# Performance work log

Measured on AMD Instinct MI355X. Metric: run time of the kernel, lower is better.

The kernel has to match this reference:

```python
import jax, jax.numpy as jnp
import numpy as np
from jax import lax

L, B, T = 512, 1024, 48


def setup_inputs() -> dict:
    key = jax.random.key(0)
    k1, k2, k3, k4, k5 = jax.random.split(key, 5)
    emissions = jax.random.normal(k1, (L, B, T), dtype=jnp.float32)
    tags = jax.random.randint(k2, (L, B), 0, T)
    mask = jnp.ones((L, B), dtype=bool)
    start_transitions = jax.random.uniform(k3, (T,), minval=-0.1, maxval=0.1, dtype=jnp.float32)
    end_transitions = jax.random.uniform(k4, (T,), minval=-0.1, maxval=0.1, dtype=jnp.float32)
    transitions = jax.random.uniform(k5, (T, T), minval=-0.1, maxval=0.1, dtype=jnp.float32)
    return {
        'emissions': emissions,
        'tags': tags,
        'mask': mask,
        'start_transitions': start_transitions,
        'end_transitions': end_transitions,
        'transitions': transitions,
    }


def reference(emissions, tags, mask, start_transitions, end_transitions, transitions):
    # emissions: [L, B, T] float; tags: [L, B] int; mask: [L, B] bool (seq-first)
    fm = mask.astype(emissions.dtype)
    seq_len, batch, _ = emissions.shape
    b_idx = jnp.arange(batch)

    # ---- numerator: score of the gold path ----
    # emission score at each step: emissions[i, b, tags[i, b]] -> [L, B]
    em_sc = jnp.take_along_axis(emissions, tags[:, :, None], axis=2)[:, :, 0]
    # transition score between consecutive tags -> [L-1, B]
    trans_sc = transitions[tags[:-1], tags[1:]]
    score = start_transitions[tags[0]] + em_sc[0]
    score = score + jnp.sum((trans_sc + em_sc[1:]) * fm[1:], axis=0)
    seq_ends = mask.astype(jnp.int32).sum(axis=0) - 1  # [B]
    last_tags = tags[seq_ends, b_idx]
    score = score + end_transitions[last_tags]

    # ---- denominator: log partition via forward algorithm (scan) ----
    alpha0 = start_transitions + emissions[0]  # [B, T]

    def step(alpha, xs):
        em, m = xs  # em: [B, T], m: [B]
        # [B, T(prev), T(next)] logsumexp over prev
        next_alpha = jax.nn.logsumexp(
            alpha[:, :, None] + transitions[None, :, :] + em[:, None, :], axis=1)
        alpha = jnp.where(m[:, None], next_alpha, alpha)
        return alpha, None

    alpha, _ = lax.scan(step, alpha0, (emissions[1:], mask[1:]))
    denominator = jax.nn.logsumexp(alpha + end_transitions, axis=1)  # [B]

    llh = score - denominator
    return jnp.mean(llh)  # reduction='mean' (default)
```

## Files before the change

kernel.cpp:

```cpp
#include <hip/hip_runtime.h>

#define LSEQ 512
#define BATCH 1024
#define T 48

typedef __fp16 h2_t __attribute__((ext_vector_type(2)));

static __device__ __forceinline__ float bcast_lane0(float x) {
    return __int_as_float(__builtin_amdgcn_readfirstlane(__float_as_int(x)));
}

static __device__ __forceinline__ float dot2acc(int pk_bits, h2_t e, float acc) {
#if __has_builtin(__builtin_amdgcn_fdot2)
    return __builtin_amdgcn_fdot2(__builtin_bit_cast(h2_t, pk_bits), e, acc, false);
#else
    h2_t a = __builtin_bit_cast(h2_t, pk_bits);
    return __builtin_fmaf((float)a.x, (float)e.x,
           __builtin_fmaf((float)a.y, (float)e.y, acc));
#endif
}

static __device__ __forceinline__ float fast_rcp(float x) {
#if __has_builtin(__builtin_amdgcn_rcpf)
    return __builtin_amdgcn_rcpf(x);
#else
    return 1.0f / x;
#endif
}

static __device__ __forceinline__ int pack_pairs(float w) {
    int wsh = __builtin_amdgcn_update_dpp(0, __float_as_int(w), 0x111, 0xF, 0xF, true);
    return __builtin_bit_cast(int, __builtin_amdgcn_cvt_pkrtz(w, __int_as_float(wsh)));
}

__global__ __launch_bounds__(256, 1) void crf_forward(
    const float* __restrict__ emissions,
    const int* __restrict__ mask,
    const float* __restrict__ start_tr,
    const float* __restrict__ end_tr,
    const float* __restrict__ trans,
    float* __restrict__ denom_out)
{
    const int wave = threadIdx.x >> 6;
    const int lane = threadIdx.x & 63;
    const int b    = blockIdx.x * 4 + wave;
    const bool valid = (lane < T);
    const int jc   = valid ? lane : (T - 1);

    h2_t Ep[T / 2];
    #pragma unroll
    for (int k = 0; k < T / 2; ++k) {
        float e0 = __expf(trans[(2 * k) * T + jc]);
        float e1 = __expf(trans[(2 * k + 1) * T + jc]);
        Ep[k] = __builtin_amdgcn_cvt_pkrtz(e0, e1);
    }

    const float a0 = start_tr[jc] + emissions[(size_t)b * T + jc];
    const float A0 = bcast_lane0(a0);
    float w = valid ? __expf(a0 - A0) : 0.f;
    float C = A0;
    int pk = pack_pairs(w);

    float em0_ = emissions[((size_t)1 * BATCH + b) * T + jc];
    float em1_ = emissions[((size_t)2 * BATCH + b) * T + jc];
    float em2_ = emissions[((size_t)3 * BATCH + b) * T + jc];
    float em3_ = emissions[((size_t)4 * BATCH + b) * T + jc];
    int   mk0_ = mask[1 * BATCH + b];
    int   mk1_ = mask[2 * BATCH + b];
    int   mk2_ = mask[3 * BATCH + b];
    int   mk3_ = mask[4 * BATCH + b];

    for (int t = 1; t <= LSEQ - 1; ++t) {
        const float em = em0_;  em0_ = em1_; em1_ = em2_; em2_ = em3_;
        const int   mk = mk0_;  mk0_ = mk1_; mk1_ = mk2_; mk2_ = mk3_;
        int tn = t + 4; if (tn > LSEQ - 1) tn = LSEQ - 1;
        em3_ = emissions[((size_t)tn * BATCH + b) * T + jc];
        mk3_ = mask[tn * BATCH + b];

        const float em0 = bcast_lane0(em);
        const float e   = __expf(em - em0);

        float acc0 = 0.f, acc1 = 0.f, acc2 = 0.f, acc3 = 0.f;
        #pragma unroll
        for (int k = 0; k < T / 2; k += 4) {
            acc0 = dot2acc(__builtin_amdgcn_readlane(pk, 2 * k + 0), Ep[k + 0], acc0);
            acc1 = dot2acc(__builtin_amdgcn_readlane(pk, 2 * k + 2), Ep[k + 1], acc1);
            acc2 = dot2acc(__builtin_amdgcn_readlane(pk, 2 * k + 4), Ep[k + 2], acc2);
            acc3 = dot2acc(__builtin_amdgcn_readlane(pk, 2 * k + 6), Ep[k + 3], acc3);
        }
        const float S  = (acc0 + acc1) + (acc2 + acc3);
        const float S0 = bcast_lane0(S);
        const float rs = fast_rcp(S0);
        const float lg = __logf(S0);
        const float wnew = (e * rs) * S;

        const bool upd = (mk != 0);
        w = (upd && valid) ? wnew : w;
        C = upd ? (C + em0 + lg) : C;

        pk = pack_pairs(w);
    }

    float v = valid ? (w * __expf(end_tr[jc])) : 0.f;
    #pragma unroll
    for (int off = 32; off > 0; off >>= 1) v += __shfl_xor(v, off);
    if (lane == 0) denom_out[b] = C + __logf(v);
}

__global__ __launch_bounds__(256) void crf_score_partial(
    const float* __restrict__ emissions,
    const int* __restrict__ tags,
    const int* __restrict__ mask,
    const float* __restrict__ trans,
    float* __restrict__ part,
    int* __restrict__ cnt,
    int csz)
{
    const int gid = blockIdx.x * blockDim.x + threadIdx.x;
    const int b = gid & (BATCH - 1);
    const int c = gid >> 10;
    const int t0 = c * csz;
    const int t1 = t0 + csz;

    float sc = 0.f;
    int ct = 0;
    const int tstart = (t0 == 0) ? 1 : t0;
    if (t0 == 0) ct += mask[b] ? 1 : 0;

    int tag_prev = tags[(tstart - 1) * BATCH + b];
    for (int t = tstart; t < t1; ++t) {
        const int tag = tags[t * BATCH + b];
        const int mt = mask[t * BATCH + b];
        if (mt) {
            sc += trans[tag_prev * T + tag]
                + emissions[((size_t)t * BATCH + b) * T + tag];
            ct += 1;
        }
        tag_prev = tag;
    }
    part[gid] = sc;
    cnt[gid] = ct;
}

__global__ __launch_bounds__(1024) void crf_combine(
    const float* __restrict__ emissions,
    const int* __restrict__ tags,
    const float* __restrict__ start_tr,
    const float* __restrict__ end_tr,
    const float* __restrict__ part,
    const int* __restrict__ cnt,
    const float* __restrict__ denom,
    float* __restrict__ out,
    int nchunk)
{
    const int b = threadIdx.x;

    const int tag0 = tags[b];
    float sc = start_tr[tag0] + emissions[(size_t)b * T + tag0];
    int ct = 0;
    for (int c = 0; c < nchunk; ++c) {
        sc += part[c * BATCH + b];
        ct += cnt[c * BATCH + b];
    }
    if (ct < 1) ct = 1;
    const int last_tag = tags[(ct - 1) * BATCH + b];
    sc += end_tr[last_tag];

    const float llh = sc - denom[b];

    __shared__ float red[1024];
    red[b] = llh;
    __syncthreads();
    #pragma unroll
    for (int s = 512; s > 0; s >>= 1) {
        if (b < s) red[b] += red[b + s];
        __syncthreads();
    }
    if (b == 0) out[0] = red[0] / (float)BATCH;
}

extern "C" void kernel_launch(void* const* d_in, const int* in_sizes, int n_in,
                              void* d_out, int out_size, void* d_ws, size_t ws_size,
                              hipStream_t stream) {
    const float* emissions        = (const float*)d_in[0];
    const int* tags               = (const int*)d_in[1];
    const int* mask               = (const int*)d_in[2];
    const float* start_tr         = (const float*)d_in[3];
    const float* end_tr           = (const float*)d_in[4];
    const float* trans            = (const float*)d_in[5];
    float* out                    = (float*)d_out;

    const int nchunk = (ws_size >= (size_t)(BATCH * 4 + 32 * BATCH * 8 + 64)) ? 32 : 8;
    const int csz    = LSEQ / nchunk;

    float* denom = (float*)d_ws;
    float* part  = denom + BATCH;
    int*   cnt   = (int*)(part + nchunk * BATCH);

    crf_forward<<<256, 256, 0, stream>>>(emissions, mask, start_tr, end_tr, trans, denom);
    crf_score_partial<<<nchunk * BATCH / 256, 256, 0, stream>>>(
        emissions, tags, mask, trans, part, cnt, csz);
    crf_combine<<<1, 1024, 0, stream>>>(emissions, tags, start_tr, end_tr,
                                        part, cnt, denom, out, nchunk);
}
```

Before: 198.0 us.

## Use fp32 FMA with LDS-resident exp(transitions) and chunked double-buffered emission prefetch

Replaces the packed-fp16 dot2 inner product with fp32 FMAs that read exp(transitions) from a padded transposed table in LDS instead of registers. Emission and mask loads become double-buffered chunks of 8 timesteps, prefetched one chunk ahead. The aim is to restore fp32 precision and hide global load latency better, at the cost of 48 LDS reads per step on top of the 48 readlanes, which may lengthen the serial per-step critical path.

```diff
diff --git a/kernel.cpp b/kernel.cpp
--- a/kernel.cpp
+++ b/kernel.cpp
@@ -3,23 +3,16 @@
 #define LSEQ 512
 #define BATCH 1024
 #define T 48
-
-typedef __fp16 h2_t __attribute__((ext_vector_type(2)));
+#define TP 49
+#define CHUNK 8
+#define NCH (LSEQ / CHUNK)
 
 static __device__ __forceinline__ float bcast_lane0(float x) {
     return __int_as_float(__builtin_amdgcn_readfirstlane(__float_as_int(x)));
 }
-
-static __device__ __forceinline__ float dot2acc(int pk_bits, h2_t e, float acc) {
-#if __has_builtin(__builtin_amdgcn_fdot2)
-    return __builtin_amdgcn_fdot2(__builtin_bit_cast(h2_t, pk_bits), e, acc, false);
-#else
-    h2_t a = __builtin_bit_cast(h2_t, pk_bits);
-    return __builtin_fmaf((float)a.x, (float)e.x,
-           __builtin_fmaf((float)a.y, (float)e.y, acc));
-#endif
-}
-
+static __device__ __forceinline__ float rl(float x, int i) {
+    return __int_as_float(__builtin_amdgcn_readlane(__float_as_int(x), i));
+}
 static __device__ __forceinline__ float fast_rcp(float x) {
 #if __has_builtin(__builtin_amdgcn_rcpf)
     return __builtin_amdgcn_rcpf(x);
@@ -28,9 +21,28 @@
 #endif
 }
 
-static __device__ __forceinline__ int pack_pairs(float w) {
-    int wsh = __builtin_amdgcn_update_dpp(0, __float_as_int(w), 0x111, 0xF, 0xF, true);
-    return __builtin_bit_cast(int, __builtin_amdgcn_cvt_pkrtz(w, __int_as_float(wsh)));
+static __device__ __forceinline__ void crf_step(
+    float& w, float& C, float em, int mk, int tt, bool valid,
+    const float* __restrict__ Ejv)
+{
+    const float em0 = bcast_lane0(em);
+    const float e   = __expf(em - em0);
+    float s0 = 0.f, s1 = 0.f, s2 = 0.f, s3 = 0.f;
+    #pragma unroll
+    for (int i = 0; i < T; i += 4) {
+        s0 = __builtin_fmaf(rl(w, i + 0), Ejv[i + 0], s0);
+        s1 = __builtin_fmaf(rl(w, i + 1), Ejv[i + 1], s1);
+        s2 = __builtin_fmaf(rl(w, i + 2), Ejv[i + 2], s2);
+        s3 = __builtin_fmaf(rl(w, i + 3), Ejv[i + 3], s3);
+    }
+    const float S    = (s0 + s1) + (s2 + s3);
+    const float S0   = bcast_lane0(S);
+    const float rs   = fast_rcp(S0);
+    const float lg   = __logf(S0);
+    const float wnew = (e * rs) * S;
+    const bool  upd  = (mk != 0) && (tt < LSEQ);
+    w = (upd && valid) ? wnew : w;
+    C = upd ? (C + em0 + lg) : C;
 }
 
 __global__ __launch_bounds__(256, 1) void crf_forward(
@@ -41,64 +53,78 @@
     const float* __restrict__ trans,
     float* __restrict__ denom_out)
 {
-    const int wave = threadIdx.x >> 6;
-    const int lane = threadIdx.x & 63;
+    __shared__ float Elds[T * TP];
+    const int tid = threadIdx.x;
+    #pragma unroll
+    for (int r = 0; r < (T * T + 255) / 256; ++r) {
+        int g = tid + r * 256;
+        if (g < T * T) {
+            int i = g / T, j = g % T;
+            Elds[j * TP + i] = __expf(trans[g]);
+        }
+    }
+    __syncthreads();
+
+    const int wave = tid >> 6, lane = tid & 63;
     const int b    = blockIdx.x * 4 + wave;
     const bool valid = (lane < T);
     const int jc   = valid ? lane : (T - 1);
-
-    h2_t Ep[T / 2];
-    #pragma unroll
-    for (int k = 0; k < T / 2; ++k) {
-        float e0 = __expf(trans[(2 * k) * T + jc]);
-        float e1 = __expf(trans[(2 * k + 1) * T + jc]);
-        Ep[k] = __builtin_amdgcn_cvt_pkrtz(e0, e1);
-    }
-
-    const float a0 = start_tr[jc] + emissions[(size_t)b * T + jc];
+    const unsigned ebase = (unsigned)(jc * TP);
+
+    const float* emb = emissions + (size_t)b * T + jc;
+    const int*   mkb = mask + b;
+
+    const float a0 = start_tr[jc] + emb[0];
     const float A0 = bcast_lane0(a0);
     float w = valid ? __expf(a0 - A0) : 0.f;
     float C = A0;
-    int pk = pack_pairs(w);
-
-    float em0_ = emissions[((size_t)1 * BATCH + b) * T + jc];
-    float em1_ = emissions[((size_t)2 * BATCH + b) * T + jc];
-    float em2_ = emissions[((size_t)3 * BATCH + b) * T + jc];
-    float em3_ = emissions[((size_t)4 * BATCH + b) * T + jc];
-    int   mk0_ = mask[1 * BATCH + b];
-    int   mk1_ = mask[2 * BATCH + b];
-    int   mk2_ = mask[3 * BATCH + b];
-    int   mk3_ = mask[4 * BATCH + b];
-
-    for (int t = 1; t <= LSEQ - 1; ++t) {
-        const float em = em0_;  em0_ = em1_; em1_ = em2_; em2_ = em3_;
-        const int   mk = mk0_;  mk0_ = mk1_; mk1_ = mk2_; mk2_ = mk3_;
-        int tn = t + 4; if (tn > LSEQ - 1) tn = LSEQ - 1;
-        em3_ = emissions[((size_t)tn * BATCH + b) * T + jc];
-        mk3_ = mask[tn * BATCH + b];
-
-        const float em0 = bcast_lane0(em);
-        const float e   = __expf(em - em0);
-
-        float acc0 = 0.f, acc1 = 0.f, acc2 = 0.f, acc3 = 0.f;
-        #pragma unroll
-        for (int k = 0; k < T / 2; k += 4) {
-            acc0 = dot2acc(__builtin_amdgcn_readlane(pk, 2 * k + 0), Ep[k + 0], acc0);
-            acc1 = dot2acc(__builtin_amdgcn_readlane(pk, 2 * k + 2), Ep[k + 1], acc1);
-            acc2 = dot2acc(__builtin_amdgcn_readlane(pk, 2 * k + 4), Ep[k + 2], acc2);
-            acc3 = dot2acc(__builtin_amdgcn_readlane(pk, 2 * k + 6), Ep[k + 3], acc3);
-        }
-        const float S  = (acc0 + acc1) + (acc2 + acc3);
-        const float S0 = bcast_lane0(S);
-        const float rs = fast_rcp(S0);
-        const float lg = __logf(S0);
-        const float wnew = (e * rs) * S;
-
-        const bool upd = (mk != 0);
-        w = (upd && valid) ? wnew : w;
-        C = upd ? (C + em0 + lg) : C;
-
-        pk = pack_pairs(w);
+
+    float emA[CHUNK], emB[CHUNK];
+    int   mkA[CHUNK], mkB[CHUNK];
+    #pragma unroll
+    for (int u = 0; u < CHUNK; ++u) {
+        const int tt = 1 + u;
+        emA[u] = emb[(size_t)tt * (BATCH * T)];
+        mkA[u] = mkb[tt * BATCH];
+    }
+
+    for (int c = 0; c < NCH; c += 2) {
+        {
+            const int tB = 1 + (c + 1) * CHUNK;
+            #pragma unroll
+            for (int u = 0; u < CHUNK; ++u) {
+                int tt = tB + u; if (tt > LSEQ - 1) tt = LSEQ - 1;
+                emB[u] = emb[(size_t)tt * (BATCH * T)];
+                mkB[u] = mkb[tt * BATCH];
+            }
+        }
+        {
+            const int t0 = 1 + c * CHUNK;
+            #pragma unroll
+            for (int u = 0; u < CHUNK; ++u) {
+                unsigned eb = ebase;
+                asm volatile("" : "+v"(eb));
+                crf_step(w, C, emA[u], mkA[u], t0 + u, valid, &Elds[eb]);
+            }
+        }
+        {
+            const int tA = 1 + (c + 2) * CHUNK;
+            #pragma unroll
+            for (int u = 0; u < CHUNK; ++u) {
+                int tt = tA + u; if (tt > LSEQ - 1) tt = LSEQ - 1;
+                emA[u] = emb[(size_t)tt * (BATCH * T)];
+                mkA[u] = mkb[tt * BATCH];
+            }
+        }
+        {
+            const int t0 = 1 + (c + 1) * CHUNK;
+            #pragma unroll
+            for (int u = 0; u < CHUNK; ++u) {
+                unsigned eb = ebase;
+                asm volatile("" : "+v"(eb));
+                crf_step(w, C, emB[u], mkB[u], t0 + u, valid, &Elds[eb]);
+            }
+        }
     }
 
     float v = valid ? (w * __expf(end_tr[jc])) : 0.f;
```

Result: slower. 224.9 us (+13.6%).

## Batch 16 sequences per wave and compute CRF forward recursion with MFMA

Applied to the files above, without the earlier changes.

The forward-algorithm kernel now processes 16 batch elements per 64-lane wave and performs the 48x48 transition matrix-vector products as 16x16x16 fp16 MFMA ops instead of per-lane dot2 with readlane broadcasts. Rescaling switches from a lane-0 reference to the per-column max, applied after the emission exponent, and the emission loads become vectorized float4 loads with a 4-slot software prefetch. This cuts the number of waves from 1024 to 64 and removes the serial readlane chain, at the cost of 9 dependent MFMAs per step and lower occupancy and parallelism across the GPU.

```diff
diff --git a/kernel.cpp b/kernel.cpp
--- a/kernel.cpp
+++ b/kernel.cpp
@@ -4,36 +4,45 @@
 #define BATCH 1024
 #define T 48
 
-typedef __fp16 h2_t __attribute__((ext_vector_type(2)));
-
-static __device__ __forceinline__ float bcast_lane0(float x) {
-    return __int_as_float(__builtin_amdgcn_readfirstlane(__float_as_int(x)));
-}
-
-static __device__ __forceinline__ float dot2acc(int pk_bits, h2_t e, float acc) {
-#if __has_builtin(__builtin_amdgcn_fdot2)
-    return __builtin_amdgcn_fdot2(__builtin_bit_cast(h2_t, pk_bits), e, acc, false);
+typedef float f4 __attribute__((ext_vector_type(4)));
+typedef __fp16 h2 __attribute__((ext_vector_type(2)));
+typedef __fp16 h4 __attribute__((ext_vector_type(4)));
+typedef float f32x4 __attribute__((ext_vector_type(4)));
+
+static __device__ __forceinline__ f32x4 mfma16(h4 a, h4 b, f32x4 c) {
+#if defined(__HIP_DEVICE_COMPILE__)
+#if __has_builtin(__builtin_amdgcn_mfma_f32_16x16x16f16)
+    return __builtin_amdgcn_mfma_f32_16x16x16f16(a, b, c, 0, 0, 0);
 #else
-    h2_t a = __builtin_bit_cast(h2_t, pk_bits);
-    return __builtin_fmaf((float)a.x, (float)e.x,
-           __builtin_fmaf((float)a.y, (float)e.y, acc));
+    return __builtin_amdgcn_mfma_f32_16x16x16_f16(a, b, c, 0, 0, 0);
 #endif
-}
-
+#else
+    return c;
+#endif
+}
+
+static __device__ __forceinline__ h4 pack4(float a, float b, float c, float d) {
+    h2 lo = __builtin_amdgcn_cvt_pkrtz(a, b);
+    h2 hi = __builtin_amdgcn_cvt_pkrtz(c, d);
+    h4 r; r.x = lo.x; r.y = lo.y; r.z = hi.x; r.w = hi.y;
+    return r;
+}
+static __device__ __forceinline__ h4 sel4(bool c, h4 a, h4 b) {
+    int2 ai = __builtin_bit_cast(int2, a), bi = __builtin_bit_cast(int2, b);
+    int2 r; r.x = c ? ai.x : bi.x; r.y = c ? ai.y : bi.y;
+    return __builtin_bit_cast(h4, r);
+}
 static __device__ __forceinline__ float fast_rcp(float x) {
-#if __has_builtin(__builtin_amdgcn_rcpf)
+#if defined(__HIP_DEVICE_COMPILE__) && __has_builtin(__builtin_amdgcn_rcpf)
     return __builtin_amdgcn_rcpf(x);
 #else
     return 1.0f / x;
 #endif
 }
 
-static __device__ __forceinline__ int pack_pairs(float w) {
-    int wsh = __builtin_amdgcn_update_dpp(0, __float_as_int(w), 0x111, 0xF, 0xF, true);
-    return __builtin_bit_cast(int, __builtin_amdgcn_cvt_pkrtz(w, __int_as_float(wsh)));
-}
-
-__global__ __launch_bounds__(256, 1) void crf_forward(
+struct Slot { f4 em[3]; int mk; };
+
+__global__ __launch_bounds__(64, 1) void crf_forward(
     const float* __restrict__ emissions,
     const int* __restrict__ mask,
     const float* __restrict__ start_tr,
@@ -41,70 +50,106 @@
     const float* __restrict__ trans,
     float* __restrict__ denom_out)
 {
-    const int wave = threadIdx.x >> 6;
-    const int lane = threadIdx.x & 63;
-    const int b    = blockIdx.x * 4 + wave;
-    const bool valid = (lane < T);
-    const int jc   = valid ? lane : (T - 1);
-
-    h2_t Ep[T / 2];
-    #pragma unroll
-    for (int k = 0; k < T / 2; ++k) {
-        float e0 = __expf(trans[(2 * k) * T + jc]);
-        float e1 = __expf(trans[(2 * k + 1) * T + jc]);
-        Ep[k] = __builtin_amdgcn_cvt_pkrtz(e0, e1);
-    }
-
-    const float a0 = start_tr[jc] + emissions[(size_t)b * T + jc];
-    const float A0 = bcast_lane0(a0);
-    float w = valid ? __expf(a0 - A0) : 0.f;
-    float C = A0;
-    int pk = pack_pairs(w);
-
-    float em0_ = emissions[((size_t)1 * BATCH + b) * T + jc];
-    float em1_ = emissions[((size_t)2 * BATCH + b) * T + jc];
-    float em2_ = emissions[((size_t)3 * BATCH + b) * T + jc];
-    float em3_ = emissions[((size_t)4 * BATCH + b) * T + jc];
-    int   mk0_ = mask[1 * BATCH + b];
-    int   mk1_ = mask[2 * BATCH + b];
-    int   mk2_ = mask[3 * BATCH + b];
-    int   mk3_ = mask[4 * BATCH + b];
-
-    for (int t = 1; t <= LSEQ - 1; ++t) {
-        const float em = em0_;  em0_ = em1_; em1_ = em2_; em2_ = em3_;
-        const int   mk = mk0_;  mk0_ = mk1_; mk1_ = mk2_; mk2_ = mk3_;
-        int tn = t + 4; if (tn > LSEQ - 1) tn = LSEQ - 1;
-        em3_ = emissions[((size_t)tn * BATCH + b) * T + jc];
-        mk3_ = mask[tn * BATCH + b];
-
-        const float em0 = bcast_lane0(em);
-        const float e   = __expf(em - em0);
-
-        float acc0 = 0.f, acc1 = 0.f, acc2 = 0.f, acc3 = 0.f;
-        #pragma unroll
-        for (int k = 0; k < T / 2; k += 4) {
-            acc0 = dot2acc(__builtin_amdgcn_readlane(pk, 2 * k + 0), Ep[k + 0], acc0);
-            acc1 = dot2acc(__builtin_amdgcn_readlane(pk, 2 * k + 2), Ep[k + 1], acc1);
-            acc2 = dot2acc(__builtin_amdgcn_readlane(pk, 2 * k + 4), Ep[k + 2], acc2);
-            acc3 = dot2acc(__builtin_amdgcn_readlane(pk, 2 * k + 6), Ep[k + 3], acc3);
+    const int lane  = threadIdx.x;
+    const int col   = lane & 15;
+    const int g     = lane >> 4;
+    const int bbase = blockIdx.x * 16;
+    const int b     = bbase + col;
+
+    h4 Af[3][3];
+    #pragma unroll
+    for (int rb = 0; rb < 3; ++rb)
+        #pragma unroll
+        for (int kc = 0; kc < 3; ++kc) {
+            float e0 = __expf(trans[(16*kc + 4*g + 0)*T + 16*rb + col]);
+            float e1 = __expf(trans[(16*kc + 4*g + 1)*T + 16*rb + col]);
+            float e2 = __expf(trans[(16*kc + 4*g + 2)*T + 16*rb + col]);
+            float e3 = __expf(trans[(16*kc + 4*g + 3)*T + 16*rb + col]);
+            Af[rb][kc] = pack4(e0, e1, e2, e3);
         }
-        const float S  = (acc0 + acc1) + (acc2 + acc3);
-        const float S0 = bcast_lane0(S);
-        const float rs = fast_rcp(S0);
-        const float lg = __logf(S0);
-        const float wnew = (e * rs) * S;
-
-        const bool upd = (mk != 0);
-        w = (upd && valid) ? wnew : w;
-        C = upd ? (C + em0 + lg) : C;
-
-        pk = pack_pairs(w);
-    }
-
-    float v = valid ? (w * __expf(end_tr[jc])) : 0.f;
-    #pragma unroll
-    for (int off = 32; off > 0; off >>= 1) v += __shfl_xor(v, off);
-    if (lane == 0) denom_out[b] = C + __logf(v);
+
+    float a[12];
+    #pragma unroll
+    for (int kc = 0; kc < 3; ++kc) {
+        const f4 em0v = *(const f4*)(emissions + (size_t)b * T + 16*kc + 4*g);
+        const f4 st4  = *(const f4*)(start_tr + 16*kc + 4*g);
+        #pragma unroll
+        for (int i = 0; i < 4; ++i) a[4*kc + i] = st4[i] + em0v[i];
+    }
+    float m = fmaxf(fmaxf(fmaxf(a[0],a[1]), fmaxf(a[2],a[3])),
+              fmaxf(fmaxf(fmaxf(a[4],a[5]), fmaxf(a[6],a[7])),
+                    fmaxf(fmaxf(a[8],a[9]), fmaxf(a[10],a[11]))));
+    m = fmaxf(m, __shfl_xor(m, 16));
+    m = fmaxf(m, __shfl_xor(m, 32));
+    float C = m;
+    h4 Bf[3];
+    #pragma unroll
+    for (int kc = 0; kc < 3; ++kc)
+        Bf[kc] = pack4(__expf(a[4*kc+0]-m), __expf(a[4*kc+1]-m),
+                       __expf(a[4*kc+2]-m), __expf(a[4*kc+3]-m));
+
+    auto step = [&](const Slot& S) {
+        const f32x4 z = {0.f, 0.f, 0.f, 0.f};
+        f32x4 D[3];
+        #pragma unroll
+        for (int rb = 0; rb < 3; ++rb) {
+            D[rb] = mfma16(Af[rb][0], Bf[0], z);
+            D[rb] = mfma16(Af[rb][1], Bf[1], D[rb]);
+            D[rb] = mfma16(Af[rb][2], Bf[2], D[rb]);
+        }
+        float y[12];
+        #pragma unroll
+        for (int kc = 0; kc < 3; ++kc)
+            #pragma unroll
+            for (int i = 0; i < 4; ++i)
+                y[4*kc + i] = __expf(S.em[kc][i]) * D[kc][i];
+        float mx = fmaxf(fmaxf(fmaxf(y[0],y[1]), fmaxf(y[2],y[3])),
+                   fmaxf(fmaxf(fmaxf(y[4],y[5]), fmaxf(y[6],y[7])),
+                         fmaxf(fmaxf(y[8],y[9]), fmaxf(y[10],y[11]))));
+        mx = fmaxf(mx, __shfl_xor(mx, 16));
+        mx = fmaxf(mx, __shfl_xor(mx, 32));
+        const float rs = fast_rcp(mx);
+        const float lg = __logf(mx);
+        const bool upd = (S.mk != 0);
+        #pragma unroll
+        for (int kc = 0; kc < 3; ++kc)
+            Bf[kc] = sel4(upd,
+                          pack4(y[4*kc+0]*rs, y[4*kc+1]*rs,
+                                y[4*kc+2]*rs, y[4*kc+3]*rs),
+                          Bf[kc]);
+        C = upd ? (C + lg) : C;
+    };
+
+    auto load = [&](Slot& S, int t) {
+        const size_t off = ((size_t)t * BATCH + b) * T + 4*g;
+        S.em[0] = *(const f4*)(emissions + off);
+        S.em[1] = *(const f4*)(emissions + off + 16);
+        S.em[2] = *(const f4*)(emissions + off + 32);
+        S.mk    = mask[t * BATCH + b];
+    };
+    auto loadc = [&](Slot& S, int t) { load(S, t > LSEQ-1 ? LSEQ-1 : t); };
+
+    Slot S0, S1, S2, S3;
+    load(S0, 1); load(S1, 2); load(S2, 3); load(S3, 4);
+    for (int t = 1; t <= LSEQ - 4; t += 4) {
+        step(S0); loadc(S0, t + 4);
+        step(S1); loadc(S1, t + 5);
+        step(S2); loadc(S2, t + 6);
+        step(S3); loadc(S3, t + 7);
+    }
+    step(S0); step(S1); step(S2);
+
+    float v = 0.f;
+    #pragma unroll
+    for (int kc = 0; kc < 3; ++kc) {
+        const f4 endv = *(const f4*)(end_tr + 16*kc + 4*g);
+        #pragma unroll
+        for (int i = 0; i < 4; ++i)
+            v += (float)Bf[kc][i] * __expf(endv[i]);
+    }
+    v += __shfl_xor(v, 16);
+    v += __shfl_xor(v, 32);
+    if (lane < 16) denom_out[bbase + lane] = C + __logf(v);
 }
 
 __global__ __launch_bounds__(256) void crf_score_partial(
@@ -197,7 +242,8 @@
     float* part  = denom + BATCH;
     int*   cnt   = (int*)(part + nchunk * BATCH);
 
-    crf_forward<<<256, 256, 0, stream>>>(emissions, mask, start_tr, end_tr, trans, denom);
+    crf_forward<<<BATCH / 16, 64, 0, stream>>>(emissions, mask, start_tr,
+                                               end_tr, trans, denom);
     crf_score_partial<<<nchunk * BATCH / 256, 256, 0, stream>>>(
         emissions, tags, mask, trans, part, cnt, csz);
     crf_combine<<<1, 1024, 0, stream>>>(emissions, tags, start_tr, end_tr,
```

Result: slower. 231.6 us (+17.0%).
